# Optimization experiments

Measured on AMD Instinct MI355X. Metric: run time of the kernel, lower is better.

## Reference

```python
import jax, jax.numpy as jnp
import numpy as np

N = 4096
D = 256
L = 4
B = 8


def _graph_norm(x, cums, gamma, beta_g, num_segments):
    # GraphNormGAT: per-graph mean / unbiased std over ragged segments.
    n = x.shape[0]
    seg = jnp.searchsorted(cums, jnp.arange(n), side='right') - 1  # [N] segment ids
    ones = jnp.ones((n,), x.dtype)
    cnt = jax.ops.segment_sum(ones, seg, num_segments=num_segments)[:, None]  # [B,1]
    mean = jax.ops.segment_sum(x, seg, num_segments=num_segments) / cnt       # [B,D]
    diff = x - mean[seg]
    var = jax.ops.segment_sum(diff * diff, seg, num_segments=num_segments) / jnp.maximum(cnt - 1.0, 1.0)
    std = jnp.sqrt(var)
    return gamma * (diff / (std[seg] + 1e-5)) + beta_g


def _mean_shift(beta, xyz, q, k, v, y_hat, mask, t, bw, use_std_att, self_distance, max_iter):
    # Distance-masked mean-shift attention: Gaussian kernel on coordinates
    # combined with QK attention; iteratively shifts xyz toward weighted mean.
    d = q.shape[-1]
    x_out = v
    for _ in range(max_iter):
        att = (q @ k.T) * (1.0 / (np.sqrt(d) * float(t)))  # [N,N]
        if use_std_att:
            m = att.mean(axis=-1, keepdims=True)
            s = att.std(axis=-1, keepdims=True)
            att = (att - m) / (s + 1e-5)
        sq = jnp.sum(xyz * xyz, axis=-1)
        d2 = jnp.maximum(sq[:, None] + sq[None, :] - 2.0 * (xyz @ xyz.T), 0.0)
        d2 = d2 + float(self_distance) * jnp.eye(xyz.shape[0], dtype=d2.dtype)
        logits = att - d2 / (2.0 * bw * bw) + jnp.log(y_hat.T + 1e-9)
        logits = jnp.where(mask, logits, -1e9)
        w = jax.nn.softmax(logits, axis=-1)  # [N,N]
        xyz = beta * (w @ xyz) + (1.0 - beta) * xyz
        x_out = w @ v
    return xyz, x_out


def setup_inputs() -> dict:
    key = jax.random.key(0)
    ks = jax.random.split(key, 12)
    inp = {}
    inp['xyz'] = jax.random.normal(ks[0], (N, 3), jnp.float32)
    inp['x'] = jax.random.normal(ks[1], (N, D), jnp.float32)
    inp['y_hat'] = jax.random.uniform(ks[2], (N, 1), jnp.float32)
    inp['distance_mask'] = jax.random.randint(ks[3], (N, N), 0, 2).astype(bool)
    inp['t'] = 1
    inp['band_width'] = jnp.ones((1,), jnp.float32)
    inp['beta'] = jax.random.uniform(ks[4], (1,), jnp.float32)
    inp['cums'] = jnp.arange(B + 1, dtype=jnp.int32) * (N // B)
    inp['big_inter_mask'] = jnp.ones((N, N), dtype=bool)
    inp['use_std_att'] = 1
    inp['self_distance'] = 10000
    scale = 1.0 / np.sqrt(D)
    inp['qw'] = jax.random.normal(ks[5], (L, D, D), jnp.float32) * scale
    inp['kw'] = jax.random.normal(ks[6], (L, D, D), jnp.float32) * scale
    inp['vw'] = jax.random.normal(ks[7], (L, D, D), jnp.float32) * scale
    inp['ow'] = jax.random.normal(ks[8], (L, D, D), jnp.float32) * scale
    inp['qb'] = jnp.zeros((L, D), jnp.float32)
    inp['kb'] = jnp.zeros((L, D), jnp.float32)
    inp['vb'] = jnp.zeros((L, D), jnp.float32)
    inp['ob'] = jnp.zeros((L, D), jnp.float32)
    inp['gamma'] = jnp.ones((L, 1, D), jnp.float32)
    inp['beta_g'] = jnp.zeros((L, 1, D), jnp.float32)
    return inp


def reference(xyz, x, y_hat, distance_mask, t, band_width, beta, cums,
              big_inter_mask, use_std_att, self_distance,
              qw, kw, vw, ow, qb, kb, vb, ob, gamma, beta_g):
    mask = distance_mask & big_inter_mask
    bw = band_width[0]
    bt = beta[0]
    for l in range(L):
        res = x
        q = x @ qw[l].T + qb[l]
        k = x @ kw[l].T + kb[l]
        v = x @ vw[l].T + vb[l]
        xyz, h = _mean_shift(bt, xyz, q, k, v, y_hat, mask, t, bw,
                             use_std_att, self_distance, max_iter=1)
        h = h @ ow[l].T + ob[l]
        x = res + h
        x = _graph_norm(x, cums, gamma[l], beta_g[l], num_segments=B)
    return x
```

## Files before the change

### kernel.cpp

```cpp
#include <hip/hip_runtime.h>
#include <hip/hip_bf16.h>
#include <math.h>

#define N_ROWS 4096
#define DIM    256
#define NLAYER 4
#define QBLK 64
#define KBLK 32
#define GN_CHUNKS 16

typedef __attribute__((ext_vector_type(8))) short bf16x8;
typedef __attribute__((ext_vector_type(4))) float f32x4;
typedef unsigned short us;

__device__ __forceinline__ us f2b(float f) {
  unsigned int u = __float_as_uint(f);
  unsigned int r = (u + 0x7fffu + ((u >> 16) & 1u)) >> 16;
  return (us)r;
}
__device__ __forceinline__ float b2f(us b) {
  return __uint_as_float(((unsigned int)b) << 16);
}

__global__ void cvt_f2b_kernel(const float* __restrict__ in,
                               us* __restrict__ out) {
  int i = blockIdx.x * 256 + threadIdx.x;
  float4 v = ((const float4*)in)[i];
  ushort4 u;
  u.x = f2b(v.x);
  u.y = f2b(v.y);
  u.z = f2b(v.z);
  u.w = f2b(v.w);
  ((ushort4*)out)[i] = u;
}

__global__ __launch_bounds__(256) void mfma_nt_kernel(
    const us* __restrict__ A, const us* __restrict__ Bm,
    const float* __restrict__ bias, const float* __restrict__ res,
    float* __restrict__ C, us* __restrict__ Cb) {
  __shared__ __align__(16) short Al[64 * 32];
  __shared__ __align__(16) short Bl[64 * 32];
  const int tid = threadIdx.x;
  const int wv = tid >> 6, lane = tid & 63;
  const int cl = lane & 15, gq = lane >> 4;
  const int wr = wv >> 1, wc = wv & 1;
  const int m0 = blockIdx.x * 64, n0 = blockIdx.y * 64;
  f32x4 acc[2][2];
#pragma unroll
  for (int mi = 0; mi < 2; ++mi)
#pragma unroll
    for (int ni = 0; ni < 2; ++ni) acc[mi][ni] = (f32x4){0.f, 0.f, 0.f, 0.f};
  for (int k0 = 0; k0 < DIM; k0 += 32) {
    __syncthreads();
    {
      int r = tid >> 2, c = tid & 3;
      *(bf16x8*)&Al[r * 32 + c * 8] =
          *(const bf16x8*)&A[(size_t)(m0 + r) * DIM + k0 + c * 8];
      *(bf16x8*)&Bl[r * 32 + c * 8] =
          *(const bf16x8*)&Bm[(size_t)(n0 + r) * DIM + k0 + c * 8];
    }
    __syncthreads();
    bf16x8 af[2], bfr[2];
#pragma unroll
    for (int mi = 0; mi < 2; ++mi)
      af[mi] = *(const bf16x8*)&Al[(wr * 32 + mi * 16 + cl) * 32 + gq * 8];
#pragma unroll
    for (int ni = 0; ni < 2; ++ni)
      bfr[ni] = *(const bf16x8*)&Bl[(wc * 32 + ni * 16 + cl) * 32 + gq * 8];
#pragma unroll
    for (int mi = 0; mi < 2; ++mi)
#pragma unroll
      for (int ni = 0; ni < 2; ++ni)
        acc[mi][ni] = __builtin_amdgcn_mfma_f32_16x16x32_bf16(
            af[mi], bfr[ni], acc[mi][ni], 0, 0, 0);
  }
#pragma unroll
  for (int mi = 0; mi < 2; ++mi)
#pragma unroll
    for (int ni = 0; ni < 2; ++ni)
#pragma unroll
      for (int i = 0; i < 4; ++i) {
        int row = m0 + wr * 32 + mi * 16 + gq * 4 + i;
        int col = n0 + wc * 32 + ni * 16 + cl;
        float v = acc[mi][ni][i];
        if (bias) v += bias[col];
        if (res) v += res[(size_t)row * DIM + col];
        C[(size_t)row * DIM + col] = v;
        if (Cb) Cb[(size_t)row * DIM + col] = f2b(v);
      }
}

__global__ __launch_bounds__(256) void mfma_qkv_kernel(
    const us* __restrict__ A, const us* __restrict__ W0,
    const us* __restrict__ W1, const us* __restrict__ W2,
    const float* __restrict__ b0, const float* __restrict__ b1,
    const float* __restrict__ b2, float* __restrict__ C0,
    float* __restrict__ C1, float* __restrict__ C2, us* __restrict__ Qb16,
    us* __restrict__ Kb16) {
  const us* Bm = (blockIdx.z == 0) ? W0 : (blockIdx.z == 1) ? W1 : W2;
  const float* bias = (blockIdx.z == 0) ? b0 : (blockIdx.z == 1) ? b1 : b2;
  float* C = (blockIdx.z == 0) ? C0 : (blockIdx.z == 1) ? C1 : C2;
  us* Cb = (blockIdx.z == 0) ? Qb16 : (blockIdx.z == 1) ? Kb16 : nullptr;
  __shared__ __align__(16) short Al[64 * 32];
  __shared__ __align__(16) short Bl[64 * 32];
  const int tid = threadIdx.x;
  const int wv = tid >> 6, lane = tid & 63;
  const int cl = lane & 15, gq = lane >> 4;
  const int wr = wv >> 1, wc = wv & 1;
  const int m0 = blockIdx.x * 64, n0 = blockIdx.y * 64;
  f32x4 acc[2][2];
#pragma unroll
  for (int mi = 0; mi < 2; ++mi)
#pragma unroll
    for (int ni = 0; ni < 2; ++ni) acc[mi][ni] = (f32x4){0.f, 0.f, 0.f, 0.f};
  for (int k0 = 0; k0 < DIM; k0 += 32) {
    __syncthreads();
    {
      int r = tid >> 2, c = tid & 3;
      *(bf16x8*)&Al[r * 32 + c * 8] =
          *(const bf16x8*)&A[(size_t)(m0 + r) * DIM + k0 + c * 8];
      *(bf16x8*)&Bl[r * 32 + c * 8] =
          *(const bf16x8*)&Bm[(size_t)(n0 + r) * DIM + k0 + c * 8];
    }
    __syncthreads();
    bf16x8 af[2], bfr[2];
#pragma unroll
    for (int mi = 0; mi < 2; ++mi)
      af[mi] = *(const bf16x8*)&Al[(wr * 32 + mi * 16 + cl) * 32 + gq * 8];
#pragma unroll
    for (int ni = 0; ni < 2; ++ni)
      bfr[ni] = *(const bf16x8*)&Bl[(wc * 32 + ni * 16 + cl) * 32 + gq * 8];
#pragma unroll
    for (int mi = 0; mi < 2; ++mi)
#pragma unroll
      for (int ni = 0; ni < 2; ++ni)
        acc[mi][ni] = __builtin_amdgcn_mfma_f32_16x16x32_bf16(
            af[mi], bfr[ni], acc[mi][ni], 0, 0, 0);
  }
#pragma unroll
  for (int mi = 0; mi < 2; ++mi)
#pragma unroll
    for (int ni = 0; ni < 2; ++ni)
#pragma unroll
      for (int i = 0; i < 4; ++i) {
        int row = m0 + wr * 32 + mi * 16 + gq * 4 + i;
        int col = n0 + wc * 32 + ni * 16 + cl;
        float v = acc[mi][ni][i] + bias[col];
        C[(size_t)row * DIM + col] = v;
        if (Cb) Cb[(size_t)row * DIM + col] = f2b(v);
      }
}

__global__ __launch_bounds__(256) void mpart_mfma_kernel(
    const us* __restrict__ Kt, float* __restrict__ Mp) {
  __shared__ __align__(16) short Al[64 * 32];
  __shared__ __align__(16) short Bl[64 * 32];
  const int tid = threadIdx.x;
  const int wv = tid >> 6, lane = tid & 63;
  const int cl = lane & 15, gq = lane >> 4;
  const int wr = wv >> 1, wc = wv & 1;
  const int a0 = blockIdx.x * 64, b0 = blockIdx.y * 64;
  const int kb = blockIdx.z * 512;
  f32x4 acc[2][2];
#pragma unroll
  for (int mi = 0; mi < 2; ++mi)
#pragma unroll
    for (int ni = 0; ni < 2; ++ni) acc[mi][ni] = (f32x4){0.f, 0.f, 0.f, 0.f};
  for (int k0 = 0; k0 < 512; k0 += 32) {
    __syncthreads();
    {
      int r = tid >> 2, c = tid & 3;
      *(bf16x8*)&Al[r * 32 + c * 8] =
          *(const bf16x8*)&Kt[(size_t)(a0 + r) * N_ROWS + kb + k0 + c * 8];
      *(bf16x8*)&Bl[r * 32 + c * 8] =
          *(const bf16x8*)&Kt[(size_t)(b0 + r) * N_ROWS + kb + k0 + c * 8];
    }
    __syncthreads();
    bf16x8 af[2], bfr[2];
#pragma unroll
    for (int mi = 0; mi < 2; ++mi)
      af[mi] = *(const bf16x8*)&Al[(wr * 32 + mi * 16 + cl) * 32 + gq * 8];
#pragma unroll
    for (int ni = 0; ni < 2; ++ni)
      bfr[ni] = *(const bf16x8*)&Bl[(wc * 32 + ni * 16 + cl) * 32 + gq * 8];
#pragma unroll
    for (int mi = 0; mi < 2; ++mi)
#pragma unroll
      for (int ni = 0; ni < 2; ++ni)
        acc[mi][ni] = __builtin_amdgcn_mfma_f32_16x16x32_bf16(
            af[mi], bfr[ni], acc[mi][ni], 0, 0, 0);
  }
#pragma unroll
  for (int mi = 0; mi < 2; ++mi)
#pragma unroll
    for (int ni = 0; ni < 2; ++ni)
#pragma unroll
      for (int i = 0; i < 4; ++i) {
        int row = a0 + wr * 32 + mi * 16 + gq * 4 + i;
        int col = b0 + wc * 32 + ni * 16 + cl;
        Mp[(size_t)blockIdx.z * 65536 + (size_t)row * DIM + col] =
            acc[mi][ni][i];
      }
}

__global__ void mreduce_kernel(const float* __restrict__ Mp,
                               float* __restrict__ Mm, us* __restrict__ Mb) {
  int e = blockIdx.x * 256 + threadIdx.x;
  float s = 0.f;
#pragma unroll
  for (int z = 0; z < 8; ++z) s += Mp[(size_t)z * 65536 + e];
  Mm[e] = s;
  Mb[e] = f2b(s);
}

__global__ void ksum_part_kernel(const float* __restrict__ K,
                                 float* __restrict__ kpart) {
  int d = threadIdx.x, b = blockIdx.x;
  float s = 0.f;
  int base = b * 64;
  for (int n = 0; n < 64; ++n) s += K[(size_t)(base + n) * DIM + d];
  kpart[b * DIM + d] = s;
}
__global__ void ksum_red_kernel(const float* __restrict__ kpart,
                                float* __restrict__ ksum) {
  int d = threadIdx.x;
  float s = 0.f;
  for (int b = 0; b < 64; ++b) s += kpart[b * DIM + d];
  ksum[d] = s;
}

__global__ __launch_bounds__(256) void stats_kernel(
    const float* __restrict__ q, const float* __restrict__ tb,
    const float* __restrict__ ksum, const int* __restrict__ tptr,
    float* __restrict__ meanv, float* __restrict__ istdv) {
  const int wave = threadIdx.x >> 6, lane = threadIdx.x & 63;
  const int row = blockIdx.x * 4 + wave;
  const float4 qv = ((const float4*)(q + (size_t)row * DIM))[lane];
  const float4 tv4 = ((const float4*)(tb + (size_t)row * DIM))[lane];
  const float4 kv = ((const float4*)ksum)[lane];
  float p1 = qv.x * kv.x + qv.y * kv.y + qv.z * kv.z + qv.w * kv.w;
  float p2 = tv4.x * qv.x + tv4.y * qv.y + tv4.z * qv.z + tv4.w * qv.w;
#pragma unroll
  for (int off = 32; off >= 1; off >>= 1) {
    p1 += __shfl_xor(p1, off);
    p2 += __shfl_xor(p2, off);
  }
  if (lane == 0) {
    float tt = (float)tptr[0];
    float sc = 1.f / (16.f * tt);
    float mean = p1 * sc * (1.f / (float)N_ROWS);
    float e2 = p2 * sc * sc * (1.f / (float)N_ROWS);
    float var = fmaxf(e2 - mean * mean, 0.f);
    meanv[row] = mean;
    istdv[row] = 1.f / (sqrtf(var) + 1e-5f);
  }
}

__global__ void prep_kernel(const float* __restrict__ yhat,
                            float* __restrict__ logy) {
  int i = blockIdx.x * 256 + threadIdx.x;
  logy[i] = logf(yhat[i] + 1e-9f);
}

__global__ void maskpack_kernel(const int* __restrict__ dmask,
                                const int* __restrict__ bmask,
                                unsigned int* __restrict__ mbits) {
  int gid = blockIdx.x * 256 + threadIdx.x;
  bool v = (dmask[gid] != 0) && (bmask[gid] != 0);
  unsigned long long bal = __ballot(v);
  if ((threadIdx.x & 63) == 0) {
    int w = gid >> 5;
    mbits[w] = (unsigned int)(bal & 0xffffffffu);
    mbits[w + 1] = (unsigned int)(bal >> 32);
  }
}

__global__ __launch_bounds__(256) void vt_kernel(const float* __restrict__ V,
                                                 us* __restrict__ Vtb) {
  __shared__ float T[64][65];
  const int n0 = blockIdx.x * 64, d0 = blockIdx.y * 64;
  const int tx = threadIdx.x & 63, ty = threadIdx.x >> 6;
#pragma unroll
  for (int p = 0; p < 16; ++p)
    T[ty + p * 4][tx] = V[(size_t)(n0 + ty + p * 4) * DIM + d0 + tx];
  __syncthreads();
#pragma unroll
  for (int p = 0; p < 16; ++p)
    Vtb[(size_t)(d0 + ty + p * 4) * N_ROWS + n0 + tx] = f2b(T[tx][ty + p * 4]);
}

__global__ __launch_bounds__(256) void flash3_kernel(
    const us* __restrict__ Qb, const us* __restrict__ Kb,
    const us* __restrict__ Vtb, const float* __restrict__ xyzc,
    const float* __restrict__ logy, const float* __restrict__ meanv,
    const float* __restrict__ istdv, const unsigned int* __restrict__ mbits,
    const int* __restrict__ tptr, const float* __restrict__ bwp,
    const int* __restrict__ usestdp, const int* __restrict__ selfdp,
    us* __restrict__ plo, us* __restrict__ phi, float* __restrict__ ps,
    float* __restrict__ paxlo, float* __restrict__ paxhi, int cps) {
  __shared__ __align__(16) short Kl[1024 * 8];
  __shared__ __align__(16) short Vtl[1024 * 8];
  __shared__ __align__(16) short Pl[4][512];

  const int tid = threadIdx.x;
  const int wv = tid >> 6, lane = tid & 63;
  const int cl = lane & 15, gq = lane >> 4;
  const int r0 = blockIdx.x * QBLK + wv * 16;
  const int split = blockIdx.y;
  const int colbase = split * cps;

  const float tv = (float)tptr[0];
  const float scale = 1.f / (16.f * tv);
  const float bw = bwp[0];
  const float inv2bw2 = 1.f / (2.f * bw * bw);
  const float t2 = 2.f * inv2bw2;
  const int usestd = usestdp[0];
  const float sd2 = (float)selfdp[0] * inv2bw2;

  bf16x8 qa[8];
  {
    const bf16x8* qp = (const bf16x8*)(Qb + (size_t)(r0 + cl) * DIM);
#pragma unroll
    for (int ks = 0; ks < 8; ++ks) qa[ks] = qp[ks * 4 + gq];
  }
  int rowg[4];
  float c1[4], cA[4], xr[4][3];
#pragma unroll
  for (int i = 0; i < 4; ++i) {
    rowg[i] = r0 + gq * 4 + i;
    float mrow = meanv[rowg[i]];
    float irow = istdv[rowg[i]];
    c1[i] = usestd ? scale * irow : scale;
    float c2 = usestd ? -mrow * irow : 0.f;
    xr[i][0] = xyzc[(size_t)rowg[i] * 3 + 0];
    xr[i][1] = xyzc[(size_t)rowg[i] * 3 + 1];
    xr[i][2] = xyzc[(size_t)rowg[i] * 3 + 2];
    float sqr = xr[i][0] * xr[i][0] + xr[i][1] * xr[i][1] + xr[i][2] * xr[i][2];
    cA[i] = c2 - sqr * inv2bw2;
  }
  float s[4] = {0.f, 0.f, 0.f, 0.f};
  float ax[4][3] = {};
  f32x4 o[16];
#pragma unroll
  for (int dt = 0; dt < 16; ++dt) o[dt] = (f32x4){0.f, 0.f, 0.f, 0.f};

  const int g0base = 2 * cl;

  for (int tt = 0; tt < cps; tt += KBLK) {
    const int t0g = colbase + tt;
    __syncthreads();
#pragma unroll
    for (int p = 0; p < 4; ++p) {
      int L = tid + p * 256;
      int ct = L >> 9, ks = (L >> 6) & 7, g = (L >> 4) & 3, c = L & 15;
      *(bf16x8*)&Kl[L * 8] =
          *(const bf16x8*)&Kb[(size_t)(t0g + 2 * c + ct) * DIM + ks * 32 +
                              g * 8];
    }
#pragma unroll
    for (int p = 0; p < 4; ++p) {
      int L = tid + p * 256;
      int dt = L >> 6, g = (L >> 4) & 3, c = L & 15;
      *(bf16x8*)&Vtl[L * 8] =
          *(const bf16x8*)&Vtb[(size_t)(dt * 16 + c) * N_ROWS + t0g + g * 8];
    }
    __syncthreads();

    int gc0 = t0g + g0base, gc1 = gc0 + 1;
    float xa0 = xyzc[(size_t)gc0 * 3 + 0];
    float xa1 = xyzc[(size_t)gc0 * 3 + 1];
    float xa2 = xyzc[(size_t)gc0 * 3 + 2];
    float xb0 = xyzc[(size_t)gc1 * 3 + 0];
    float xb1 = xyzc[(size_t)gc1 * 3 + 1];
    float xb2 = xyzc[(size_t)gc1 * 3 + 2];
    float B0 = logy[gc0] - (xa0 * xa0 + xa1 * xa1 + xa2 * xa2) * inv2bw2;
    float B1 = logy[gc1] - (xb0 * xb0 + xb1 * xb1 + xb2 * xb2) * inv2bw2;

    f32x4 st0 = (f32x4){0.f, 0.f, 0.f, 0.f};
    f32x4 st1 = (f32x4){0.f, 0.f, 0.f, 0.f};
#pragma unroll
    for (int ks = 0; ks < 8; ++ks) {
      bf16x8 kf0 = *(const bf16x8*)&Kl[(ks * 64 + gq * 16 + cl) * 8];
      st0 = __builtin_amdgcn_mfma_f32_16x16x32_bf16(qa[ks], kf0, st0, 0, 0, 0);
    }
#pragma unroll
    for (int ks = 0; ks < 8; ++ks) {
      bf16x8 kf1 = *(const bf16x8*)&Kl[(512 + ks * 64 + gq * 16 + cl) * 8];
      st1 = __builtin_amdgcn_mfma_f32_16x16x32_bf16(qa[ks], kf1, st1, 0, 0, 0);
    }

#pragma unroll
    for (int i = 0; i < 4; ++i) {
      unsigned int mw = mbits[((size_t)rowg[i] << 7) + (t0g >> 5)];
      unsigned int pb = (mw >> g0base) & 3u;
      float d30 = xr[i][0] * xa0 + xr[i][1] * xa1 + xr[i][2] * xa2;
      float d31 = xr[i][0] * xb0 + xr[i][1] * xb1 + xr[i][2] * xb2;
      float lg0 = fmaf(st0[i], c1[i], cA[i] + B0) + t2 * d30;
      float lg1 = fmaf(st1[i], c1[i], cA[i] + B1) + t2 * d31;
      if (rowg[i] == gc0) lg0 -= sd2;
      if (rowg[i] == gc1) lg1 -= sd2;
      lg0 = (pb & 1u) ? lg0 : -60.f;
      lg1 = (pb & 2u) ? lg1 : -60.f;
      float p0 = __expf(lg0);
      float p1 = __expf(lg1);
      s[i] += p0 + p1;
      ax[i][0] += p0 * xa0 + p1 * xb0;
      ax[i][1] += p0 * xa1 + p1 * xb1;
      ax[i][2] += p0 * xa2 + p1 * xb2;
      unsigned int pk = (unsigned int)f2b(p0) | ((unsigned int)f2b(p1) << 16);
      *(unsigned int*)&Pl[wv][((cl >> 2) * 16 + gq * 4 + i) * 8 +
                              (cl & 3) * 2] = pk;
    }
    bf16x8 pf = *(const bf16x8*)&Pl[wv][(gq * 16 + cl) * 8];
#pragma unroll
    for (int dt = 0; dt < 16; ++dt) {
      bf16x8 vf = *(const bf16x8*)&Vtl[(dt * 64 + gq * 16 + cl) * 8];
      o[dt] = __builtin_amdgcn_mfma_f32_16x16x32_bf16(pf, vf, o[dt], 0, 0, 0);
    }
  }

#pragma unroll
  for (int i = 0; i < 4; ++i) {
    float v = s[i];
    v += __shfl_xor(v, 1);
    v += __shfl_xor(v, 2);
    v += __shfl_xor(v, 4);
    v += __shfl_xor(v, 8);
    s[i] = v;
#pragma unroll
    for (int c = 0; c < 3; ++c) {
      float a = ax[i][c];
      a += __shfl_xor(a, 1);
      a += __shfl_xor(a, 2);
      a += __shfl_xor(a, 4);
      a += __shfl_xor(a, 8);
      ax[i][c] = a;
    }
  }
  us* pb = (split < 8) ? plo : phi;
  float* paxb = (split < 8) ? paxlo : paxhi;
  const int sl = split & 7;
  if (cl == 0) {
#pragma unroll
    for (int i = 0; i < 4; ++i) {
      ps[(size_t)split * N_ROWS + rowg[i]] = s[i];
      paxb[((size_t)sl * N_ROWS + rowg[i]) * 3 + 0] = ax[i][0];
      paxb[((size_t)sl * N_ROWS + rowg[i]) * 3 + 1] = ax[i][1];
      paxb[((size_t)sl * N_ROWS + rowg[i]) * 3 + 2] = ax[i][2];
    }
  }
#pragma unroll
  for (int dt = 0; dt < 16; ++dt)
#pragma unroll
    for (int i = 0; i < 4; ++i)
      pb[((size_t)sl * N_ROWS + rowg[i]) * DIM + dt * 16 + cl] =
          f2b(o[dt][i]);
}

__global__ __launch_bounds__(256) void merge_kernel(
    const us* __restrict__ plo, const us* __restrict__ phi,
    const float* __restrict__ ps, const float* __restrict__ paxlo,
    const float* __restrict__ paxhi, const float* __restrict__ xyzc,
    const float* __restrict__ betap, us* __restrict__ xattb,
    float* __restrict__ xyz_out, int nsplit) {
  const int wvl = threadIdx.x >> 6, lane = threadIdx.x & 63;
  const int row = blockIdx.x * 4 + wvl;
  float den = 0.f;
  for (int k = 0; k < nsplit; ++k) den += ps[(size_t)k * N_ROWS + row];
  float inv = 1.f / den;
  float a0 = 0.f, a1 = 0.f, a2 = 0.f, a3 = 0.f;
  for (int k = 0; k < nsplit; ++k) {
    const us* pb = (k < 8) ? plo : phi;
    const us* p = &pb[((size_t)(k & 7) * N_ROWS + row) * DIM + lane * 4];
    uint2 u = *(const uint2*)p;
    a0 += __uint_as_float((u.x & 0xffffu) << 16);
    a1 += __uint_as_float(u.x & 0xffff0000u);
    a2 += __uint_as_float((u.y & 0xffffu) << 16);
    a3 += __uint_as_float(u.y & 0xffff0000u);
  }
  ushort4 ov;
  ov.x = f2b(a0 * inv);
  ov.y = f2b(a1 * inv);
  ov.z = f2b(a2 * inv);
  ov.w = f2b(a3 * inv);
  *(ushort4*)&xattb[(size_t)row * DIM + lane * 4] = ov;
  if (lane < 3) {
    float axs = 0.f;
    for (int k = 0; k < nsplit; ++k) {
      const float* paxb = (k < 8) ? paxlo : paxhi;
      axs += paxb[((size_t)(k & 7) * N_ROWS + row) * 3 + lane];
    }
    float beta = betap[0];
    xyz_out[(size_t)row * 3 + lane] =
        beta * axs * inv + (1.f - beta) * xyzc[(size_t)row * 3 + lane];
  }
}

__global__ __launch_bounds__(256) void gn_part_kernel(
    const float* __restrict__ X, const int* __restrict__ cums,
    float* __restrict__ gpart) {
  const int seg = blockIdx.x, chunk = blockIdx.y, d = threadIdx.x;
  const int r0 = cums[seg], r1 = cums[seg + 1];
  const int cnt = r1 - r0;
  const int per = (cnt + GN_CHUNKS - 1) / GN_CHUNKS;
  const int a = r0 + chunk * per;
  const int b = min(a + per, r1);
  float s = 0.f, ss = 0.f;
  for (int r = a; r < b; ++r) {
    float v = X[(size_t)r * DIM + d];
    s += v;
    ss += v * v;
  }
  gpart[(((size_t)seg * GN_CHUNKS + chunk) * 2 + 0) * DIM + d] = s;
  gpart[(((size_t)seg * GN_CHUNKS + chunk) * 2 + 1) * DIM + d] = ss;
}

__global__ void gn_red_kernel(const float* __restrict__ gpart,
                              const int* __restrict__ cums,
                              float* __restrict__ gm, float* __restrict__ gi) {
  const int seg = blockIdx.x, d = threadIdx.x;
  float s = 0.f, ss = 0.f;
#pragma unroll
  for (int c = 0; c < GN_CHUNKS; ++c) {
    s += gpart[(((size_t)seg * GN_CHUNKS + c) * 2 + 0) * DIM + d];
    ss += gpart[(((size_t)seg * GN_CHUNKS + c) * 2 + 1) * DIM + d];
  }
  float cnt = (float)(cums[seg + 1] - cums[seg]);
  float mean = s / fmaxf(cnt, 1.f);
  float var = (ss - cnt * mean * mean) / fmaxf(cnt - 1.f, 1.f);
  gm[seg * DIM + d] = mean;
  gi[seg * DIM + d] = 1.f / (sqrtf(fmaxf(var, 0.f)) + 1e-5f);
}

__global__ __launch_bounds__(256) void gn_apply_kernel(
    const float* __restrict__ X, const float* __restrict__ gamma,
    const float* __restrict__ betag, const int* __restrict__ cums, int nseg,
    const float* __restrict__ gm, const float* __restrict__ gi,
    float* __restrict__ Xout, us* __restrict__ Xb, float* __restrict__ ofinal) {
  int idx = blockIdx.x * 256 + threadIdx.x;
  int base = idx * 4;
  int row = base >> 8, d0 = base & 255;
  int seg = 0;
  for (int b = 1; b <= nseg; ++b) seg += (row >= cums[b]) ? 1 : 0;
  float4 x = ((const float4*)X)[idx];
  float xs[4] = {x.x, x.y, x.z, x.w};
  const float* gmp = gm + seg * DIM + d0;
  const float* gip = gi + seg * DIM + d0;
  float o[4];
#pragma unroll
  for (int c = 0; c < 4; ++c)
    o[c] = gamma[d0 + c] * (xs[c] - gmp[c]) * gip[c] + betag[d0 + c];
  float4 ov = {o[0], o[1], o[2], o[3]};
  ((float4*)Xout)[idx] = ov;
  ushort4 ub;
  ub.x = f2b(o[0]);
  ub.y = f2b(o[1]);
  ub.z = f2b(o[2]);
  ub.w = f2b(o[3]);
  ((ushort4*)Xb)[idx] = ub;
  if (ofinal) ((float4*)ofinal)[idx] = ov;
}

extern "C" void kernel_launch(void* const* d_in, const int* in_sizes, int n_in,
                              void* d_out, int out_size, void* d_ws,
                              size_t ws_size, hipStream_t stream) {
  const float* xyz0 = (const float*)d_in[0];
  const float* x0 = (const float*)d_in[1];
  const float* yhat = (const float*)d_in[2];
  const int* dmask = (const int*)d_in[3];
  const int* tptr = (const int*)d_in[4];
  const float* bwp = (const float*)d_in[5];
  const float* betap = (const float*)d_in[6];
  const int* cums = (const int*)d_in[7];
  const int* bmask = (const int*)d_in[8];
  const int* usestdp = (const int*)d_in[9];
  const int* selfdp = (const int*)d_in[10];
  const float* qw = (const float*)d_in[11];
  const float* kw = (const float*)d_in[12];
  const float* vw = (const float*)d_in[13];
  const float* ow = (const float*)d_in[14];
  const float* qbv = (const float*)d_in[15];
  const float* kbv = (const float*)d_in[16];
  const float* vbv = (const float*)d_in[17];
  const float* obv = (const float*)d_in[18];
  const float* gamma = (const float*)d_in[19];
  const float* betag = (const float*)d_in[20];
  float* out = (float*)d_out;
  float* ws = (float*)d_ws;

  const size_t ND = (size_t)N_ROWS * DIM;
  const size_t WSZ = (size_t)NLAYER * DIM * DIM;
  float* bq = ws + 0 * ND;
  float* bk = ws + 1 * ND;
  float* bv = ws + 2 * ND;
  float* bt = ws + 3 * ND;
  float* bh = ws + 4 * ND;
  float* bx = ws + 5 * ND;
  float* Mp = ws + 6 * ND;
  float* Mm = Mp + 8 * 65536;
  float* kpart = Mm + 65536;
  float* ksum = kpart + 64 * 256;
  float* meanv = ksum + 256;
  float* istdv = meanv + 4096;
  float* gm = istdv + 4096;
  float* gi = gm + 8 * 256;
  float* logy = gi + 8 * 256;
  float* xyzA = logy + 4096;
  float* xyzB = xyzA + 3 * N_ROWS;
  unsigned int* mbits = (unsigned int*)(xyzB + 3 * N_ROWS);
  float* psbase = (float*)(mbits + (size_t)N_ROWS * 128);
  float* paxlo = psbase + 16 * (size_t)N_ROWS;
  float* gpart = paxlo + 8 * (size_t)N_ROWS * 3;
  us* Mb16 = (us*)(gpart + 8 * GN_CHUNKS * 2 * DIM);
  us* qwb = Mb16 + 65536;
  us* kwb = qwb + WSZ;
  us* vwb = kwb + WSZ;
  us* owb = vwb + WSZ;
  us* xinb = owb + WSZ;
  us* xattb = xinb + ND;
  float* compact_end = (float*)(xattb + ND);
  us* phi = (us*)compact_end;
  float* paxhi = (float*)(phi + 8 * ND);
  float* full_end = paxhi + 8 * (size_t)N_ROWS * 3;
  const size_t full_bytes = (size_t)((char*)full_end - (char*)ws);
  const int nsplit = (ws_size >= full_bytes) ? 16 : 8;
  const int cps = N_ROWS / nsplit;

  us* plo = (us*)ws;
  us* Qb16 = (us*)bh;
  us* Kb16 = Qb16 + ND;
  us* Ktb = (us*)bt;
  us* Vtb = (us*)Mp;
  float* bo = bv;

  const int nseg = in_sizes[7] - 1;

  prep_kernel<<<16, 256, 0, stream>>>(yhat, logy);
  maskpack_kernel<<<65536, 256, 0, stream>>>(dmask, bmask, mbits);
  cvt_f2b_kernel<<<256, 256, 0, stream>>>(qw, qwb);
  cvt_f2b_kernel<<<256, 256, 0, stream>>>(kw, kwb);
  cvt_f2b_kernel<<<256, 256, 0, stream>>>(vw, vwb);
  cvt_f2b_kernel<<<256, 256, 0, stream>>>(ow, owb);
  cvt_f2b_kernel<<<1024, 256, 0, stream>>>(x0, xinb);

  for (int l = 0; l < NLAYER; ++l) {
    const float* xin = (l == 0) ? x0 : bx;
    const float* xyz_in = (l == 0) ? xyz0 : ((l & 1) ? xyzB : xyzA);
    float* xyz_o = (l & 1) ? xyzA : xyzB;
    const size_t wo = (size_t)l * DIM * DIM;

    mfma_qkv_kernel<<<dim3(64, 4, 3), 256, 0, stream>>>(
        xinb, qwb + wo, kwb + wo, vwb + wo, qbv + l * DIM, kbv + l * DIM,
        vbv + l * DIM, bq, bk, bv, Qb16, Kb16);
    ksum_part_kernel<<<64, 256, 0, stream>>>(bk, kpart);
    ksum_red_kernel<<<1, 256, 0, stream>>>(kpart, ksum);
    vt_kernel<<<dim3(64, 4), 256, 0, stream>>>(bk, Ktb);
    mpart_mfma_kernel<<<dim3(4, 4, 8), 256, 0, stream>>>(Ktb, Mp);
    mreduce_kernel<<<256, 256, 0, stream>>>(Mp, Mm, Mb16);
    mfma_nt_kernel<<<dim3(64, 4), 256, 0, stream>>>(Qb16, Mb16, nullptr,
                                                    nullptr, bt, nullptr);
    stats_kernel<<<1024, 256, 0, stream>>>(bq, bt, ksum, tptr, meanv, istdv);
    vt_kernel<<<dim3(64, 4), 256, 0, stream>>>(bv, Vtb);
    flash3_kernel<<<dim3(64, nsplit), 256, 0, stream>>>(
        Qb16, Kb16, Vtb, xyz_in, logy, meanv, istdv, mbits, tptr, bwp, usestdp,
        selfdp, plo, phi, psbase, paxlo, paxhi, cps);
    merge_kernel<<<1024, 256, 0, stream>>>(plo, phi, psbase, paxlo, paxhi,
                                           xyz_in, betap, xattb, xyz_o,
                                           nsplit);
    mfma_nt_kernel<<<dim3(64, 4), 256, 0, stream>>>(xattb, owb + wo,
                                                    obv + l * DIM, xin, bo,
                                                    nullptr);
    gn_part_kernel<<<dim3(nseg, GN_CHUNKS), 256, 0, stream>>>(bo, cums, gpart);
    gn_red_kernel<<<nseg, 256, 0, stream>>>(gpart, cums, gm, gi);
    gn_apply_kernel<<<1024, 256, 0, stream>>>(
        bo, gamma + (size_t)l * DIM, betag + (size_t)l * DIM, cums, nseg, gm,
        gi, bx, xinb, (l == NLAYER - 1) ? out : nullptr);
  }
}
```

Baseline: 654.3 us.

## Fold distance terms into augmented QK/V columns and enlarge flash tiles

Q and K rows are padded to 288 columns so that the xyz dot-product term is computed inside the QK MFMA. V is augmented with xyz and a ones column, which lets the PV MFMA also produce the softmax denominator and the weighted xyz sums. The flash kernel now processes 128 rows per block, two 16-row tiles per wave, with launch bounds of 2. Separate fp32-to-bf16 conversion kernels are removed; GEMMs convert fp32 inputs while loading tiles, and the K and V transposes are merged into one launch. The per-row coefficients move into the stats kernel. The workspace layout is reorganised, and precision changes slightly because the xyz terms now pass through bf16.

After: 777.0 us. 1.19x slower.

```diff
diff --git a/kernel.cpp b/kernel.cpp
--- a/kernel.cpp
+++ b/kernel.cpp
@@ -4,9 +4,8 @@
 
 #define N_ROWS 4096
 #define DIM    256
+#define LDQ    288
 #define NLAYER 4
-#define QBLK 64
-#define KBLK 32
 #define GN_CHUNKS 16
 
 typedef __attribute__((ext_vector_type(8))) short bf16x8;
@@ -21,23 +20,23 @@
 __device__ __forceinline__ float b2f(us b) {
   return __uint_as_float(((unsigned int)b) << 16);
 }
-
-__global__ void cvt_f2b_kernel(const float* __restrict__ in,
-                               us* __restrict__ out) {
-  int i = blockIdx.x * 256 + threadIdx.x;
-  float4 v = ((const float4*)in)[i];
-  ushort4 u;
-  u.x = f2b(v.x);
-  u.y = f2b(v.y);
-  u.z = f2b(v.z);
-  u.w = f2b(v.w);
-  ((ushort4*)out)[i] = u;
+__device__ __forceinline__ bf16x8 f8_to_b8(float4 a, float4 b) {
+  bf16x8 r;
+  r[0] = (short)f2b(a.x);
+  r[1] = (short)f2b(a.y);
+  r[2] = (short)f2b(a.z);
+  r[3] = (short)f2b(a.w);
+  r[4] = (short)f2b(b.x);
+  r[5] = (short)f2b(b.y);
+  r[6] = (short)f2b(b.z);
+  r[7] = (short)f2b(b.w);
+  return r;
 }
 
 __global__ __launch_bounds__(256) void mfma_nt_kernel(
-    const us* __restrict__ A, const us* __restrict__ Bm,
-    const float* __restrict__ bias, const float* __restrict__ res,
-    float* __restrict__ C, us* __restrict__ Cb) {
+    const us* __restrict__ A, int lda, const us* __restrict__ Bb,
+    const float* __restrict__ Bf, const float* __restrict__ bias,
+    const float* __restrict__ res, float* __restrict__ C) {
   __shared__ __align__(16) short Al[64 * 32];
   __shared__ __align__(16) short Bl[64 * 32];
   const int tid = threadIdx.x;
@@ -55,9 +54,16 @@
     {
       int r = tid >> 2, c = tid & 3;
       *(bf16x8*)&Al[r * 32 + c * 8] =
-          *(const bf16x8*)&A[(size_t)(m0 + r) * DIM + k0 + c * 8];
-      *(bf16x8*)&Bl[r * 32 + c * 8] =
-          *(const bf16x8*)&Bm[(size_t)(n0 + r) * DIM + k0 + c * 8];
+          *(const bf16x8*)&A[(size_t)(m0 + r) * lda + k0 + c * 8];
+      if (Bf) {
+        float4 u = *(const float4*)&Bf[(size_t)(n0 + r) * DIM + k0 + c * 8];
+        float4 v =
+            *(const float4*)&Bf[(size_t)(n0 + r) * DIM + k0 + c * 8 + 4];
+        *(bf16x8*)&Bl[r * 32 + c * 8] = f8_to_b8(u, v);
+      } else {
+        *(bf16x8*)&Bl[r * 32 + c * 8] =
+            *(const bf16x8*)&Bb[(size_t)(n0 + r) * DIM + k0 + c * 8];
+      }
     }
     __syncthreads();
     bf16x8 af[2], bfr[2];
@@ -86,21 +92,19 @@
         if (bias) v += bias[col];
         if (res) v += res[(size_t)row * DIM + col];
         C[(size_t)row * DIM + col] = v;
-        if (Cb) Cb[(size_t)row * DIM + col] = f2b(v);
       }
 }
 
 __global__ __launch_bounds__(256) void mfma_qkv_kernel(
-    const us* __restrict__ A, const us* __restrict__ W0,
-    const us* __restrict__ W1, const us* __restrict__ W2,
+    const float* __restrict__ A, const float* __restrict__ W0,
+    const float* __restrict__ W1, const float* __restrict__ W2,
     const float* __restrict__ b0, const float* __restrict__ b1,
-    const float* __restrict__ b2, float* __restrict__ C0,
-    float* __restrict__ C1, float* __restrict__ C2, us* __restrict__ Qb16,
-    us* __restrict__ Kb16) {
-  const us* Bm = (blockIdx.z == 0) ? W0 : (blockIdx.z == 1) ? W1 : W2;
+    const float* __restrict__ b2, us* __restrict__ O0, us* __restrict__ O1,
+    us* __restrict__ O2) {
+  const float* Bm = (blockIdx.z == 0) ? W0 : (blockIdx.z == 1) ? W1 : W2;
   const float* bias = (blockIdx.z == 0) ? b0 : (blockIdx.z == 1) ? b1 : b2;
-  float* C = (blockIdx.z == 0) ? C0 : (blockIdx.z == 1) ? C1 : C2;
-  us* Cb = (blockIdx.z == 0) ? Qb16 : (blockIdx.z == 1) ? Kb16 : nullptr;
+  us* Ob = (blockIdx.z == 0) ? O0 : (blockIdx.z == 1) ? O1 : O2;
+  const int ldo = (blockIdx.z == 2) ? DIM : LDQ;
   __shared__ __align__(16) short Al[64 * 32];
   __shared__ __align__(16) short Bl[64 * 32];
   const int tid = threadIdx.x;
@@ -117,10 +121,12 @@
     __syncthreads();
     {
       int r = tid >> 2, c = tid & 3;
-      *(bf16x8*)&Al[r * 32 + c * 8] =
-          *(const bf16x8*)&A[(size_t)(m0 + r) * DIM + k0 + c * 8];
-      *(bf16x8*)&Bl[r * 32 + c * 8] =
-          *(const bf16x8*)&Bm[(size_t)(n0 + r) * DIM + k0 + c * 8];
+      float4 ua = *(const float4*)&A[(size_t)(m0 + r) * DIM + k0 + c * 8];
+      float4 va = *(const float4*)&A[(size_t)(m0 + r) * DIM + k0 + c * 8 + 4];
+      *(bf16x8*)&Al[r * 32 + c * 8] = f8_to_b8(ua, va);
+      float4 ub = *(const float4*)&Bm[(size_t)(n0 + r) * DIM + k0 + c * 8];
+      float4 vb = *(const float4*)&Bm[(size_t)(n0 + r) * DIM + k0 + c * 8 + 4];
+      *(bf16x8*)&Bl[r * 32 + c * 8] = f8_to_b8(ub, vb);
     }
     __syncthreads();
     bf16x8 af[2], bfr[2];
@@ -145,9 +151,7 @@
       for (int i = 0; i < 4; ++i) {
         int row = m0 + wr * 32 + mi * 16 + gq * 4 + i;
         int col = n0 + wc * 32 + ni * 16 + cl;
-        float v = acc[mi][ni][i] + bias[col];
-        C[(size_t)row * DIM + col] = v;
-        if (Cb) Cb[(size_t)row * DIM + col] = f2b(v);
+        Ob[(size_t)row * ldo + col] = f2b(acc[mi][ni][i] + bias[col]);
       }
 }
 
@@ -204,21 +208,20 @@
 }
 
 __global__ void mreduce_kernel(const float* __restrict__ Mp,
-                               float* __restrict__ Mm, us* __restrict__ Mb) {
+                               us* __restrict__ Mb) {
   int e = blockIdx.x * 256 + threadIdx.x;
   float s = 0.f;
 #pragma unroll
   for (int z = 0; z < 8; ++z) s += Mp[(size_t)z * 65536 + e];
-  Mm[e] = s;
   Mb[e] = f2b(s);
 }
 
-__global__ void ksum_part_kernel(const float* __restrict__ K,
+__global__ void ksum_part_kernel(const us* __restrict__ K,
                                  float* __restrict__ kpart) {
   int d = threadIdx.x, b = blockIdx.x;
   float s = 0.f;
   int base = b * 64;
-  for (int n = 0; n < 64; ++n) s += K[(size_t)(base + n) * DIM + d];
+  for (int n = 0; n < 64; ++n) s += b2f(K[(size_t)(base + n) * LDQ + d]);
   kpart[b * DIM + d] = s;
 }
 __global__ void ksum_red_kernel(const float* __restrict__ kpart,
@@ -230,29 +233,65 @@
 }
 
 __global__ __launch_bounds__(256) void stats_kernel(
-    const float* __restrict__ q, const float* __restrict__ tb,
-    const float* __restrict__ ksum, const int* __restrict__ tptr,
-    float* __restrict__ meanv, float* __restrict__ istdv) {
+    us* __restrict__ Qh, us* __restrict__ Kh, us* __restrict__ Vtb,
+    const float* __restrict__ tb, const float* __restrict__ ksum,
+    const float* __restrict__ xyzc, const float* __restrict__ logy,
+    const int* __restrict__ tptr, const float* __restrict__ bwp,
+    const int* __restrict__ usestdp, float* __restrict__ c1a,
+    float* __restrict__ cAa, float* __restrict__ colB) {
   const int wave = threadIdx.x >> 6, lane = threadIdx.x & 63;
   const int row = blockIdx.x * 4 + wave;
-  const float4 qv = ((const float4*)(q + (size_t)row * DIM))[lane];
+  ushort4 q4 = *(const ushort4*)&Qh[(size_t)row * LDQ + lane * 4];
+  float qx = b2f(q4.x), qy = b2f(q4.y), qz = b2f(q4.z), qw = b2f(q4.w);
   const float4 tv4 = ((const float4*)(tb + (size_t)row * DIM))[lane];
   const float4 kv = ((const float4*)ksum)[lane];
-  float p1 = qv.x * kv.x + qv.y * kv.y + qv.z * kv.z + qv.w * kv.w;
-  float p2 = tv4.x * qv.x + tv4.y * qv.y + tv4.z * qv.z + tv4.w * qv.w;
+  float p1 = qx * kv.x + qy * kv.y + qz * kv.z + qw * kv.w;
+  float p2 = tv4.x * qx + tv4.y * qy + tv4.z * qz + tv4.w * qw;
 #pragma unroll
   for (int off = 32; off >= 1; off >>= 1) {
     p1 += __shfl_xor(p1, off);
     p2 += __shfl_xor(p2, off);
   }
+  float tt = (float)tptr[0];
+  float sc = 1.f / (16.f * tt);
+  float mean = p1 * sc * (1.f / (float)N_ROWS);
+  float e2 = p2 * sc * sc * (1.f / (float)N_ROWS);
+  float var = fmaxf(e2 - mean * mean, 0.f);
+  float istd = 1.f / (sqrtf(var) + 1e-5f);
+  int usestd = usestdp[0];
+  float c1 = usestd ? sc * istd : sc;
+  float c2 = usestd ? -mean * istd : 0.f;
+  float bw = bwp[0];
+  float i2 = 1.f / (2.f * bw * bw);
+  float t2 = 2.f * i2;
+  float x0 = xyzc[(size_t)row * 3 + 0];
+  float x1 = xyzc[(size_t)row * 3 + 1];
+  float x2 = xyzc[(size_t)row * 3 + 2];
+  float sq = x0 * x0 + x1 * x1 + x2 * x2;
   if (lane == 0) {
-    float tt = (float)tptr[0];
-    float sc = 1.f / (16.f * tt);
-    float mean = p1 * sc * (1.f / (float)N_ROWS);
-    float e2 = p2 * sc * sc * (1.f / (float)N_ROWS);
-    float var = fmaxf(e2 - mean * mean, 0.f);
-    meanv[row] = mean;
-    istdv[row] = 1.f / (sqrtf(var) + 1e-5f);
+    c1a[row] = c1;
+    cAa[row] = c2 - sq * i2;
+    colB[row] = logy[row] - sq * i2;
+  }
+  float qs = t2 / c1;
+  if (lane < 32) {
+    float v = (lane == 0) ? qs * x0
+              : (lane == 1) ? qs * x1
+              : (lane == 2) ? qs * x2
+                            : 0.f;
+    Qh[(size_t)row * LDQ + 256 + lane] = (lane < 3) ? f2b(v) : 0;
+  } else {
+    int j = lane - 32;
+    float v = (j == 0) ? x0 : (j == 1) ? x1 : (j == 2) ? x2 : 0.f;
+    Kh[(size_t)row * LDQ + 256 + j] = (j < 3) ? f2b(v) : 0;
+  }
+  if (lane < 16) {
+    us v = 0;
+    if (lane == 0) v = f2b(x0);
+    else if (lane == 1) v = f2b(x1);
+    else if (lane == 2) v = f2b(x2);
+    else if (lane == 3) v = 0x3F80;
+    Vtb[(size_t)(256 + lane) * N_ROWS + row] = v;
   }
 }
 
@@ -275,186 +314,160 @@
   }
 }
 
-__global__ __launch_bounds__(256) void vt_kernel(const float* __restrict__ V,
-                                                 us* __restrict__ Vtb) {
-  __shared__ float T[64][65];
+__global__ __launch_bounds__(256) void vt2_kernel(const us* __restrict__ inK,
+                                                  const us* __restrict__ inV,
+                                                  us* __restrict__ outK,
+                                                  us* __restrict__ outV) {
+  __shared__ us T[64][68];
+  const us* in = (blockIdx.z == 0) ? inK : inV;
+  us* out = (blockIdx.z == 0) ? outK : outV;
+  const int lda = (blockIdx.z == 0) ? LDQ : DIM;
   const int n0 = blockIdx.x * 64, d0 = blockIdx.y * 64;
   const int tx = threadIdx.x & 63, ty = threadIdx.x >> 6;
 #pragma unroll
   for (int p = 0; p < 16; ++p)
-    T[ty + p * 4][tx] = V[(size_t)(n0 + ty + p * 4) * DIM + d0 + tx];
+    T[ty + p * 4][tx] = in[(size_t)(n0 + ty + p * 4) * lda + d0 + tx];
   __syncthreads();
 #pragma unroll
   for (int p = 0; p < 16; ++p)
-    Vtb[(size_t)(d0 + ty + p * 4) * N_ROWS + n0 + tx] = f2b(T[tx][ty + p * 4]);
-}
-
-__global__ __launch_bounds__(256) void flash3_kernel(
-    const us* __restrict__ Qb, const us* __restrict__ Kb,
-    const us* __restrict__ Vtb, const float* __restrict__ xyzc,
-    const float* __restrict__ logy, const float* __restrict__ meanv,
-    const float* __restrict__ istdv, const unsigned int* __restrict__ mbits,
-    const int* __restrict__ tptr, const float* __restrict__ bwp,
-    const int* __restrict__ usestdp, const int* __restrict__ selfdp,
-    us* __restrict__ plo, us* __restrict__ phi, float* __restrict__ ps,
-    float* __restrict__ paxlo, float* __restrict__ paxhi, int cps) {
-  __shared__ __align__(16) short Kl[1024 * 8];
-  __shared__ __align__(16) short Vtl[1024 * 8];
-  __shared__ __align__(16) short Pl[4][512];
+    out[(size_t)(d0 + ty + p * 4) * N_ROWS + n0 + tx] = T[tx][ty + p * 4];
+}
+
+__global__ __launch_bounds__(256, 2) void flash5_kernel(
+    const us* __restrict__ Qh, const us* __restrict__ Kh,
+    const us* __restrict__ Vtb, const float* __restrict__ colB,
+    const float* __restrict__ c1a, const float* __restrict__ cAa,
+    const unsigned int* __restrict__ mbits, const float* __restrict__ bwp,
+    const int* __restrict__ selfdp, us* __restrict__ plo, us* __restrict__ phi,
+    float* __restrict__ ps, float* __restrict__ paxlo,
+    float* __restrict__ paxhi, int cps) {
+  __shared__ __align__(16) short Khl[1152 * 8];
+  __shared__ __align__(16) short Vhl[1088 * 8];
+  __shared__ __align__(16) short Pl[8][512];
 
   const int tid = threadIdx.x;
   const int wv = tid >> 6, lane = tid & 63;
   const int cl = lane & 15, gq = lane >> 4;
-  const int r0 = blockIdx.x * QBLK + wv * 16;
+  const int R0 = blockIdx.x * 128 + wv * 32;
   const int split = blockIdx.y;
   const int colbase = split * cps;
 
-  const float tv = (float)tptr[0];
-  const float scale = 1.f / (16.f * tv);
   const float bw = bwp[0];
-  const float inv2bw2 = 1.f / (2.f * bw * bw);
-  const float t2 = 2.f * inv2bw2;
-  const int usestd = usestdp[0];
-  const float sd2 = (float)selfdp[0] * inv2bw2;
-
-  bf16x8 qa[8];
-  {
-    const bf16x8* qp = (const bf16x8*)(Qb + (size_t)(r0 + cl) * DIM);
-#pragma unroll
-    for (int ks = 0; ks < 8; ++ks) qa[ks] = qp[ks * 4 + gq];
-  }
-  int rowg[4];
-  float c1[4], cA[4], xr[4][3];
-#pragma unroll
-  for (int i = 0; i < 4; ++i) {
-    rowg[i] = r0 + gq * 4 + i;
-    float mrow = meanv[rowg[i]];
-    float irow = istdv[rowg[i]];
-    c1[i] = usestd ? scale * irow : scale;
-    float c2 = usestd ? -mrow * irow : 0.f;
-    xr[i][0] = xyzc[(size_t)rowg[i] * 3 + 0];
-    xr[i][1] = xyzc[(size_t)rowg[i] * 3 + 1];
-    xr[i][2] = xyzc[(size_t)rowg[i] * 3 + 2];
-    float sqr = xr[i][0] * xr[i][0] + xr[i][1] * xr[i][1] + xr[i][2] * xr[i][2];
-    cA[i] = c2 - sqr * inv2bw2;
-  }
-  float s[4] = {0.f, 0.f, 0.f, 0.f};
-  float ax[4][3] = {};
-  f32x4 o[16];
-#pragma unroll
-  for (int dt = 0; dt < 16; ++dt) o[dt] = (f32x4){0.f, 0.f, 0.f, 0.f};
-
-  const int g0base = 2 * cl;
-
-  for (int tt = 0; tt < cps; tt += KBLK) {
+  const float i2 = 1.f / (2.f * bw * bw);
+  const float sd2 = (float)selfdp[0] * i2;
+
+  bf16x8 qa[2][9];
+#pragma unroll
+  for (int rt = 0; rt < 2; ++rt) {
+    const bf16x8* qp = (const bf16x8*)(Qh + (size_t)(R0 + rt * 16 + cl) * LDQ);
+#pragma unroll
+    for (int ks = 0; ks < 9; ++ks) qa[rt][ks] = qp[ks * 4 + gq];
+  }
+  float c1v[2][4], cAv[2][4];
+#pragma unroll
+  for (int rt = 0; rt < 2; ++rt)
+#pragma unroll
+    for (int i = 0; i < 4; ++i) {
+      int row = R0 + rt * 16 + gq * 4 + i;
+      c1v[rt][i] = c1a[row];
+      cAv[rt][i] = cAa[row];
+    }
+  f32x4 o[2][17];
+#pragma unroll
+  for (int rt = 0; rt < 2; ++rt)
+#pragma unroll
+    for (int dt = 0; dt < 17; ++dt) o[rt][dt] = (f32x4){0.f, 0.f, 0.f, 0.f};
+
+  for (int tt = 0; tt < cps; tt += 32) {
     const int t0g = colbase + tt;
     __syncthreads();
 #pragma unroll
-    for (int p = 0; p < 4; ++p) {
+    for (int p = 0; p < 9; ++p) {
       int L = tid + p * 256;
-      int ct = L >> 9, ks = (L >> 6) & 7, g = (L >> 4) & 3, c = L & 15;
-      *(bf16x8*)&Kl[L * 8] =
-          *(const bf16x8*)&Kb[(size_t)(t0g + 2 * c + ct) * DIM + ks * 32 +
-                              g * 8];
-    }
-#pragma unroll
-    for (int p = 0; p < 4; ++p) {
-      int L = tid + p * 256;
-      int dt = L >> 6, g = (L >> 4) & 3, c = L & 15;
-      *(bf16x8*)&Vtl[L * 8] =
-          *(const bf16x8*)&Vtb[(size_t)(dt * 16 + c) * N_ROWS + t0g + g * 8];
-    }
-    __syncthreads();
-
-    int gc0 = t0g + g0base, gc1 = gc0 + 1;
-    float xa0 = xyzc[(size_t)gc0 * 3 + 0];
-    float xa1 = xyzc[(size_t)gc0 * 3 + 1];
-    float xa2 = xyzc[(size_t)gc0 * 3 + 2];
-    float xb0 = xyzc[(size_t)gc1 * 3 + 0];
-    float xb1 = xyzc[(size_t)gc1 * 3 + 1];
-    float xb2 = xyzc[(size_t)gc1 * 3 + 2];
-    float B0 = logy[gc0] - (xa0 * xa0 + xa1 * xa1 + xa2 * xa2) * inv2bw2;
-    float B1 = logy[gc1] - (xb0 * xb0 + xb1 * xb1 + xb2 * xb2) * inv2bw2;
-
-    f32x4 st0 = (f32x4){0.f, 0.f, 0.f, 0.f};
-    f32x4 st1 = (f32x4){0.f, 0.f, 0.f, 0.f};
-#pragma unroll
-    for (int ks = 0; ks < 8; ++ks) {
-      bf16x8 kf0 = *(const bf16x8*)&Kl[(ks * 64 + gq * 16 + cl) * 8];
-      st0 = __builtin_amdgcn_mfma_f32_16x16x32_bf16(qa[ks], kf0, st0, 0, 0, 0);
-    }
-#pragma unroll
-    for (int ks = 0; ks < 8; ++ks) {
-      bf16x8 kf1 = *(const bf16x8*)&Kl[(512 + ks * 64 + gq * 16 + cl) * 8];
-      st1 = __builtin_amdgcn_mfma_f32_16x16x32_bf16(qa[ks], kf1, st1, 0, 0, 0);
-    }
-
-#pragma unroll
-    for (int i = 0; i < 4; ++i) {
-      unsigned int mw = mbits[((size_t)rowg[i] << 7) + (t0g >> 5)];
-      unsigned int pb = (mw >> g0base) & 3u;
-      float d30 = xr[i][0] * xa0 + xr[i][1] * xa1 + xr[i][2] * xa2;
-      float d31 = xr[i][0] * xb0 + xr[i][1] * xb1 + xr[i][2] * xb2;
-      float lg0 = fmaf(st0[i], c1[i], cA[i] + B0) + t2 * d30;
-      float lg1 = fmaf(st1[i], c1[i], cA[i] + B1) + t2 * d31;
-      if (rowg[i] == gc0) lg0 -= sd2;
-      if (rowg[i] == gc1) lg1 -= sd2;
-      lg0 = (pb & 1u) ? lg0 : -60.f;
-      lg1 = (pb & 2u) ? lg1 : -60.f;
-      float p0 = __expf(lg0);
-      float p1 = __expf(lg1);
-      s[i] += p0 + p1;
-      ax[i][0] += p0 * xa0 + p1 * xb0;
-      ax[i][1] += p0 * xa1 + p1 * xb1;
-      ax[i][2] += p0 * xa2 + p1 * xb2;
-      unsigned int pk = (unsigned int)f2b(p0) | ((unsigned int)f2b(p1) << 16);
-      *(unsigned int*)&Pl[wv][((cl >> 2) * 16 + gq * 4 + i) * 8 +
-                              (cl & 3) * 2] = pk;
-    }
-    bf16x8 pf = *(const bf16x8*)&Pl[wv][(gq * 16 + cl) * 8];
-#pragma unroll
-    for (int dt = 0; dt < 16; ++dt) {
-      bf16x8 vf = *(const bf16x8*)&Vtl[(dt * 64 + gq * 16 + cl) * 8];
-      o[dt] = __builtin_amdgcn_mfma_f32_16x16x32_bf16(pf, vf, o[dt], 0, 0, 0);
-    }
-  }
-
-#pragma unroll
-  for (int i = 0; i < 4; ++i) {
-    float v = s[i];
-    v += __shfl_xor(v, 1);
-    v += __shfl_xor(v, 2);
-    v += __shfl_xor(v, 4);
-    v += __shfl_xor(v, 8);
-    s[i] = v;
-#pragma unroll
-    for (int c = 0; c < 3; ++c) {
-      float a = ax[i][c];
-      a += __shfl_xor(a, 1);
-      a += __shfl_xor(a, 2);
-      a += __shfl_xor(a, 4);
-      a += __shfl_xor(a, 8);
-      ax[i][c] = a;
-    }
-  }
+      if (L < 1152) {
+        int ks = L >> 7, ct = (L >> 6) & 1, g = (L >> 4) & 3, c = L & 15;
+        *(bf16x8*)&Khl[L * 8] =
+            *(const bf16x8*)&Kh[(size_t)(t0g + 2 * c + ct) * LDQ + ks * 32 +
+                                g * 8];
+      } else if (L < 2240) {
+        int L2 = L - 1152;
+        int dt = L2 >> 6, g = (L2 >> 4) & 3, c = L2 & 15;
+        *(bf16x8*)&Vhl[L2 * 8] =
+            *(const bf16x8*)&Vtb[(size_t)(dt * 16 + c) * N_ROWS + t0g + g * 8];
+      }
+    }
+    __syncthreads();
+
+    const int gc0 = t0g + 2 * cl;
+    const float cb0 = colB[gc0];
+    const float cb1 = colB[gc0 + 1];
+
+#pragma unroll
+    for (int rt = 0; rt < 2; ++rt) {
+      f32x4 s0 = (f32x4){0.f, 0.f, 0.f, 0.f};
+      f32x4 s1 = (f32x4){0.f, 0.f, 0.f, 0.f};
+#pragma unroll
+      for (int ks = 0; ks < 9; ++ks) {
+        bf16x8 kf = *(const bf16x8*)&Khl[(ks * 128 + gq * 16 + cl) * 8];
+        s0 = __builtin_amdgcn_mfma_f32_16x16x32_bf16(qa[rt][ks], kf, s0, 0, 0,
+                                                     0);
+      }
+#pragma unroll
+      for (int ks = 0; ks < 9; ++ks) {
+        bf16x8 kf = *(const bf16x8*)&Khl[(ks * 128 + 64 + gq * 16 + cl) * 8];
+        s1 = __builtin_amdgcn_mfma_f32_16x16x32_bf16(qa[rt][ks], kf, s1, 0, 0,
+                                                     0);
+      }
+#pragma unroll
+      for (int i = 0; i < 4; ++i) {
+        int row = R0 + rt * 16 + gq * 4 + i;
+        unsigned int mw = mbits[((size_t)row << 7) + (t0g >> 5)];
+        unsigned int pm = (mw >> (2 * cl)) & 3u;
+        float lg0 = fmaf(s0[i], c1v[rt][i], cAv[rt][i] + cb0);
+        float lg1 = fmaf(s1[i], c1v[rt][i], cAv[rt][i] + cb1);
+        if (row == gc0) lg0 -= sd2;
+        if (row == gc0 + 1) lg1 -= sd2;
+        lg0 = (pm & 1u) ? lg0 : -60.f;
+        lg1 = (pm & 2u) ? lg1 : -60.f;
+        float p0 = __expf(lg0);
+        float p1 = __expf(lg1);
+        unsigned int pk =
+            (unsigned int)f2b(p0) | ((unsigned int)f2b(p1) << 16);
+        *(unsigned int*)&Pl[wv * 2 + rt]
+                          [((cl >> 2) * 16 + gq * 4 + i) * 8 + (cl & 3) * 2] =
+            pk;
+      }
+    }
+    bf16x8 pf0 = *(const bf16x8*)&Pl[wv * 2 + 0][(gq * 16 + cl) * 8];
+    bf16x8 pf1 = *(const bf16x8*)&Pl[wv * 2 + 1][(gq * 16 + cl) * 8];
+#pragma unroll
+    for (int dt = 0; dt < 17; ++dt) {
+      bf16x8 vf = *(const bf16x8*)&Vhl[(dt * 64 + gq * 16 + cl) * 8];
+      o[0][dt] = __builtin_amdgcn_mfma_f32_16x16x32_bf16(pf0, vf, o[0][dt], 0,
+                                                         0, 0);
+      o[1][dt] = __builtin_amdgcn_mfma_f32_16x16x32_bf16(pf1, vf, o[1][dt], 0,
+                                                         0, 0);
+    }
+  }
+
   us* pb = (split < 8) ? plo : phi;
   float* paxb = (split < 8) ? paxlo : paxhi;
   const int sl = split & 7;
-  if (cl == 0) {
+#pragma unroll
+  for (int rt = 0; rt < 2; ++rt)
 #pragma unroll
     for (int i = 0; i < 4; ++i) {
-      ps[(size_t)split * N_ROWS + rowg[i]] = s[i];
-      paxb[((size_t)sl * N_ROWS + rowg[i]) * 3 + 0] = ax[i][0];
-      paxb[((size_t)sl * N_ROWS + rowg[i]) * 3 + 1] = ax[i][1];
-      paxb[((size_t)sl * N_ROWS + rowg[i]) * 3 + 2] = ax[i][2];
-    }
-  }
-#pragma unroll
-  for (int dt = 0; dt < 16; ++dt)
-#pragma unroll
-    for (int i = 0; i < 4; ++i)
-      pb[((size_t)sl * N_ROWS + rowg[i]) * DIM + dt * 16 + cl] =
-          f2b(o[dt][i]);
+      int row = R0 + rt * 16 + gq * 4 + i;
+#pragma unroll
+      for (int dt = 0; dt < 16; ++dt)
+        pb[((size_t)sl * N_ROWS + row) * DIM + dt * 16 + cl] =
+            f2b(o[rt][dt][i]);
+      float aug = o[rt][16][i];
+      if (cl < 3)
+        paxb[((size_t)sl * N_ROWS + row) * 3 + cl] = aug;
+      else if (cl == 3)
+        ps[(size_t)split * N_ROWS + row] = aug;
+    }
 }
 
 __global__ __launch_bounds__(256) void merge_kernel(
@@ -469,6 +482,7 @@
   for (int k = 0; k < nsplit; ++k) den += ps[(size_t)k * N_ROWS + row];
   float inv = 1.f / den;
   float a0 = 0.f, a1 = 0.f, a2 = 0.f, a3 = 0.f;
+  float axs = 0.f;
   for (int k = 0; k < nsplit; ++k) {
     const us* pb = (k < 8) ? plo : phi;
     const us* p = &pb[((size_t)(k & 7) * N_ROWS + row) * DIM + lane * 4];
@@ -477,6 +491,10 @@
     a1 += __uint_as_float(u.x & 0xffff0000u);
     a2 += __uint_as_float((u.y & 0xffffu) << 16);
     a3 += __uint_as_float(u.y & 0xffff0000u);
+    if (lane < 3) {
+      const float* paxb = (k < 8) ? paxlo : paxhi;
+      axs += paxb[((size_t)(k & 7) * N_ROWS + row) * 3 + lane];
+    }
   }
   ushort4 ov;
   ov.x = f2b(a0 * inv);
@@ -485,11 +503,6 @@
   ov.w = f2b(a3 * inv);
   *(ushort4*)&xattb[(size_t)row * DIM + lane * 4] = ov;
   if (lane < 3) {
-    float axs = 0.f;
-    for (int k = 0; k < nsplit; ++k) {
-      const float* paxb = (k < 8) ? paxlo : paxhi;
-      axs += paxb[((size_t)(k & 7) * N_ROWS + row) * 3 + lane];
-    }
     float beta = betap[0];
     xyz_out[(size_t)row * 3 + lane] =
         beta * axs * inv + (1.f - beta) * xyzc[(size_t)row * 3 + lane];
@@ -536,7 +549,7 @@
     const float* __restrict__ X, const float* __restrict__ gamma,
     const float* __restrict__ betag, const int* __restrict__ cums, int nseg,
     const float* __restrict__ gm, const float* __restrict__ gi,
-    float* __restrict__ Xout, us* __restrict__ Xb, float* __restrict__ ofinal) {
+    float* __restrict__ Xout, float* __restrict__ ofinal) {
   int idx = blockIdx.x * 256 + threadIdx.x;
   int base = idx * 4;
   int row = base >> 8, d0 = base & 255;
@@ -552,12 +565,6 @@
     o[c] = gamma[d0 + c] * (xs[c] - gmp[c]) * gip[c] + betag[d0 + c];
   float4 ov = {o[0], o[1], o[2], o[3]};
   ((float4*)Xout)[idx] = ov;
-  ushort4 ub;
-  ub.x = f2b(o[0]);
-  ub.y = f2b(o[1]);
-  ub.z = f2b(o[2]);
-  ub.w = f2b(o[3]);
-  ((ushort4*)Xb)[idx] = ub;
   if (ofinal) ((float4*)ofinal)[idx] = ov;
 }
 
@@ -589,59 +596,45 @@
   float* ws = (float*)d_ws;
 
   const size_t ND = (size_t)N_ROWS * DIM;
-  const size_t WSZ = (size_t)NLAYER * DIM * DIM;
-  float* bq = ws + 0 * ND;
-  float* bk = ws + 1 * ND;
-  float* bv = ws + 2 * ND;
-  float* bt = ws + 3 * ND;
-  float* bh = ws + 4 * ND;
-  float* bx = ws + 5 * ND;
-  float* Mp = ws + 6 * ND;
-  float* Mm = Mp + 8 * 65536;
-  float* kpart = Mm + 65536;
-  float* ksum = kpart + 64 * 256;
-  float* meanv = ksum + 256;
-  float* istdv = meanv + 4096;
-  float* gm = istdv + 4096;
-  float* gi = gm + 8 * 256;
-  float* logy = gi + 8 * 256;
-  float* xyzA = logy + 4096;
+
+  us* Vb16 = (us*)ws;
+  float* bt = ws;
+  us* plo = (us*)ws;
+  us* Qh = (us*)(ws + 4 * ND);
+  us* Kh = Qh + (size_t)N_ROWS * LDQ;
+  us* Vtb = Kh + (size_t)N_ROWS * LDQ;
+  unsigned int* mbits = (unsigned int*)(Vtb + (size_t)272 * N_ROWS);
+  float* kpart = (float*)(mbits + (size_t)N_ROWS * 128);
+  float* ksum = kpart + 64 * DIM;
+  float* c1a = ksum + DIM;
+  float* cAa = c1a + N_ROWS;
+  float* colB = cAa + N_ROWS;
+  float* logy = colB + N_ROWS;
+  float* xyzA = logy + N_ROWS;
   float* xyzB = xyzA + 3 * N_ROWS;
-  unsigned int* mbits = (unsigned int*)(xyzB + 3 * N_ROWS);
-  float* psbase = (float*)(mbits + (size_t)N_ROWS * 128);
+  float* gm = xyzB + 3 * N_ROWS;
+  float* gi = gm + 8 * DIM;
+  float* gpart = gi + 8 * DIM;
+  float* psbase = gpart + 8 * GN_CHUNKS * 2 * DIM;
   float* paxlo = psbase + 16 * (size_t)N_ROWS;
-  float* gpart = paxlo + 8 * (size_t)N_ROWS * 3;
-  us* Mb16 = (us*)(gpart + 8 * GN_CHUNKS * 2 * DIM);
-  us* qwb = Mb16 + 65536;
-  us* kwb = qwb + WSZ;
-  us* vwb = kwb + WSZ;
-  us* owb = vwb + WSZ;
-  us* xinb = owb + WSZ;
-  us* xattb = xinb + ND;
-  float* compact_end = (float*)(xattb + ND);
-  us* phi = (us*)compact_end;
-  float* paxhi = (float*)(phi + 8 * ND);
-  float* full_end = paxhi + 8 * (size_t)N_ROWS * 3;
-  const size_t full_bytes = (size_t)((char*)full_end - (char*)ws);
-  const int nsplit = (ws_size >= full_bytes) ? 16 : 8;
+  float* paxhi = paxlo + 8 * (size_t)N_ROWS * 3;
+  us* Mb16 = (us*)(paxhi + 8 * (size_t)N_ROWS * 3);
+  float* Pend = (float*)(Mb16 + 65536);
+  float* bo = Pend;
+  us* Ktb = (us*)(bo + ND);
+  float* Mp = (float*)(Ktb + (size_t)256 * N_ROWS);
+  us* phi = (us*)Pend;
+  us* xattb = Ktb;
+  const size_t P0w = (size_t)(Pend - ws);
+  const size_t full16 = (P0w + 5 * ND) * 4;
+  const int nsplit = (ws_size >= full16) ? 16 : 8;
   const int cps = N_ROWS / nsplit;
-
-  us* plo = (us*)ws;
-  us* Qb16 = (us*)bh;
-  us* Kb16 = Qb16 + ND;
-  us* Ktb = (us*)bt;
-  us* Vtb = (us*)Mp;
-  float* bo = bv;
+  float* bx = Pend + (size_t)(nsplit == 16 ? 4 : 2) * ND;
 
   const int nseg = in_sizes[7] - 1;
 
   prep_kernel<<<16, 256, 0, stream>>>(yhat, logy);
   maskpack_kernel<<<65536, 256, 0, stream>>>(dmask, bmask, mbits);
-  cvt_f2b_kernel<<<256, 256, 0, stream>>>(qw, qwb);
-  cvt_f2b_kernel<<<256, 256, 0, stream>>>(kw, kwb);
-  cvt_f2b_kernel<<<256, 256, 0, stream>>>(vw, vwb);
-  cvt_f2b_kernel<<<256, 256, 0, stream>>>(ow, owb);
-  cvt_f2b_kernel<<<1024, 256, 0, stream>>>(x0, xinb);
 
   for (int l = 0; l < NLAYER; ++l) {
     const float* xin = (l == 0) ? x0 : bx;
@@ -650,30 +643,29 @@
     const size_t wo = (size_t)l * DIM * DIM;
 
     mfma_qkv_kernel<<<dim3(64, 4, 3), 256, 0, stream>>>(
-        xinb, qwb + wo, kwb + wo, vwb + wo, qbv + l * DIM, kbv + l * DIM,
-        vbv + l * DIM, bq, bk, bv, Qb16, Kb16);
-    ksum_part_kernel<<<64, 256, 0, stream>>>(bk, kpart);
+        xin, qw + wo, kw + wo, vw + wo, qbv + l * DIM, kbv + l * DIM,
+        vbv + l * DIM, Qh, Kh, Vb16);
+    ksum_part_kernel<<<64, 256, 0, stream>>>(Kh, kpart);
+    vt2_kernel<<<dim3(64, 4, 2), 256, 0, stream>>>(Kh, Vb16, Ktb, Vtb);
     ksum_red_kernel<<<1, 256, 0, stream>>>(kpart, ksum);
-    vt_kernel<<<dim3(64, 4), 256, 0, stream>>>(bk, Ktb);
     mpart_mfma_kernel<<<dim3(4, 4, 8), 256, 0, stream>>>(Ktb, Mp);
-    mreduce_kernel<<<256, 256, 0, stream>>>(Mp, Mm, Mb16);
-    mfma_nt_kernel<<<dim3(64, 4), 256, 0, stream>>>(Qb16, Mb16, nullptr,
-                                                    nullptr, bt, nullptr);
-    stats_kernel<<<1024, 256, 0, stream>>>(bq, bt, ksum, tptr, meanv, istdv);
-    vt_kernel<<<dim3(64, 4), 256, 0, stream>>>(bv, Vtb);
-    flash3_kernel<<<dim3(64, nsplit), 256, 0, stream>>>(
-        Qb16, Kb16, Vtb, xyz_in, logy, meanv, istdv, mbits, tptr, bwp, usestdp,
-        selfdp, plo, phi, psbase, paxlo, paxhi, cps);
+    mreduce_kernel<<<256, 256, 0, stream>>>(Mp, Mb16);
+    mfma_nt_kernel<<<dim3(64, 4), 256, 0, stream>>>(Qh, LDQ, Mb16, nullptr,
+                                                    nullptr, nullptr, bt);
+    stats_kernel<<<1024, 256, 0, stream>>>(Qh, Kh, Vtb, bt, ksum, xyz_in, logy,
+                                           tptr, bwp, usestdp, c1a, cAa, colB);
+    flash5_kernel<<<dim3(32, nsplit), 256, 0, stream>>>(
+        Qh, Kh, Vtb, colB, c1a, cAa, mbits, bwp, selfdp, plo, phi, psbase,
+        paxlo, paxhi, cps);
     merge_kernel<<<1024, 256, 0, stream>>>(plo, phi, psbase, paxlo, paxhi,
                                            xyz_in, betap, xattb, xyz_o,
                                            nsplit);
-    mfma_nt_kernel<<<dim3(64, 4), 256, 0, stream>>>(xattb, owb + wo,
-                                                    obv + l * DIM, xin, bo,
-                                                    nullptr);
+    mfma_nt_kernel<<<dim3(64, 4), 256, 0, stream>>>(
+        xattb, DIM, nullptr, ow + wo, obv + l * DIM, xin, bo);
     gn_part_kernel<<<dim3(nseg, GN_CHUNKS), 256, 0, stream>>>(bo, cums, gpart);
     gn_red_kernel<<<nseg, 256, 0, stream>>>(gpart, cums, gm, gi);
     gn_apply_kernel<<<1024, 256, 0, stream>>>(
         bo, gamma + (size_t)l * DIM, betag + (size_t)l * DIM, cums, nseg, gm,
-        gi, bx, xinb, (l == NLAYER - 1) ? out : nullptr);
-  }
-}
+        gi, bx, (l == NLAYER - 1) ? out : nullptr);
+  }
+}
```
